# Optimization experiments

Hardware: AMD Instinct MI355X
Metric: run time of the kernel (lower is better)

## Reference

```python
import jax, jax.numpy as jnp
import numpy as np


def _chamfer(src, tgt):
    # src: [B, N, 3], tgt: [B, M, 3]
    x2 = jnp.sum(src * src, axis=-1)              # [B, N]
    y2 = jnp.sum(tgt * tgt, axis=-1)              # [B, M]
    xy = jnp.einsum('bnd,bmd->bnm', src, tgt)     # [B, N, M]
    d2 = x2[:, :, None] + y2[:, None, :] - 2.0 * xy
    d2 = jnp.maximum(d2, 0.0)                     # guard tiny negatives
    cham_x = jnp.min(d2, axis=2)                  # [B, N] min over tgt
    cham_y = jnp.min(d2, axis=1)                  # [B, M] min over src
    # point_reduction='mean', batch_reduction='sum'
    loss = jnp.sum(jnp.mean(cham_x, axis=1)) + jnp.sum(jnp.mean(cham_y, axis=1))
    return loss


def setup_inputs() -> dict:
    key = jax.random.key(0)
    k1, k2 = jax.random.split(key)
    src = jax.random.normal(k1, (16, 4096, 3), dtype=jnp.float32)
    tgt = jax.random.normal(k2, (16, 4096, 3), dtype=jnp.float32)
    return {"src": src, "tgt": tgt}


def reference(src, tgt):
    wgeo = 1.0
    return wgeo * _chamfer(src, tgt)
```

## Files before the change

### kernel.cpp

```cpp
#include <hip/hip_runtime.h>
#include <hip/hip_bf16.h>


#define BATCH   16
#define NPTS    4096
#define CHUNKC  1024
#define NCHUNKS (NPTS / CHUNKC)
#define NSTRIPS 16
#define NSTEP   (CHUNKC / 64)

typedef __attribute__((ext_vector_type(8)))  short short8;
typedef __attribute__((ext_vector_type(16))) float float16;

union U4S8 { uint4 u; short8 s; };

__device__ inline unsigned int bfb(float v) {
    __hip_bfloat16 h = __float2bfloat16(v);
    unsigned short u; __builtin_memcpy(&u, &h, 2);
    return (unsigned int)u;
}
__device__ inline float bff(float v) { return __bfloat162float(__float2bfloat16(v)); }

#define ONEB 0x3F80u

__device__ inline void buildA(float x, float y, float z, uint4& w0, uint4& w1) {
    float xhf = bff(x), yhf = bff(y), zhf = bff(z);
    float f = fmaf(x, x, fmaf(y, y, z * z));
    float fhf = bff(f);
    unsigned xh = bfb(xhf), yh = bfb(yhf), zh = bfb(zhf);
    unsigned xl = bfb(x - xhf), yl = bfb(y - yhf), zl = bfb(z - zhf);
    unsigned fh = bfb(fhf), fl = bfb(f - fhf);
    w0 = make_uint4(xh | (yh << 16), zh | (xh << 16),
                    yh | (zh << 16), xl | (yl << 16));
    w1 = make_uint4(zl | (fh << 16), fl | (ONEB << 16), ONEB, 0u);
}

__device__ inline void buildB(float x, float y, float z, uint4& w0, uint4& w1) {
    float xhf = bff(x), yhf = bff(y), zhf = bff(z);
    float f = fmaf(x, x, fmaf(y, y, z * z));
    float fhf = bff(f);
    unsigned a = bfb(-2.0f * xhf), b = bfb(-2.0f * yhf), c = bfb(-2.0f * zhf);
    unsigned d = bfb(-2.0f * (x - xhf)), e = bfb(-2.0f * (y - yhf)),
             g = bfb(-2.0f * (z - zhf));
    unsigned fh = bfb(fhf), fl = bfb(f - fhf);
    w0 = make_uint4(a | (b << 16), c | (d << 16),
                    e | (g << 16), a | (b << 16));
    w1 = make_uint4(c | (ONEB << 16), ONEB | (fh << 16), fl, 0u);
}

__global__ __launch_bounds__(256, 2) void chamfer_kernel(
    const float* __restrict__ src, const float* __restrict__ tgt,
    float* __restrict__ out)
{
    __shared__ uint4 sbuf[2][2][CHUNKC];
    __shared__ float wsum[4];

    int blk = blockIdx.x;
    const int strip = blk & (NSTRIPS - 1); blk >>= 4;
    const int b     = blk & 15;            blk >>= 4;
    const int dir   = blk;

    const int t    = threadIdx.x;
    const int lane = t & 63;
    const int w    = t >> 6;
    const int half = lane >> 5;
    const int l5   = lane & 31;

    const float* Araw = (dir ? tgt : src) + (size_t)b * NPTS * 3;
    const float* Braw = (dir ? src : tgt) + (size_t)b * NPTS * 3;

    short8 afr[2];
#pragma unroll
    for (int g = 0; g < 2; g++) {
        int row = strip * 256 + g * 128 + w * 32 + l5;
        uint4 w0, w1;
        buildA(Araw[3 * row], Araw[3 * row + 1], Araw[3 * row + 2], w0, w1);
        U4S8 tt; tt.u = half ? w1 : w0;
        afr[g] = tt.s;
    }

    float nx[4][3];
    auto loadRaw = [&](int c) {
#pragma unroll
        for (int k = 0; k < 4; k++) {
            int p = c * CHUNKC + t + k * 256;
            nx[k][0] = Braw[3 * p + 0];
            nx[k][1] = Braw[3 * p + 1];
            nx[k][2] = Braw[3 * p + 2];
        }
    };
    auto convertWrite = [&](int bi) {
#pragma unroll
        for (int k = 0; k < 4; k++) {
            int lp = t + k * 256;
            uint4 w0, w1;
            buildB(nx[k][0], nx[k][1], nx[k][2], w0, w1);
            sbuf[bi][0][lp] = w0;
            sbuf[bi][1][lp] = w1;
        }
    };

    const float16 z16 = {0.f,0.f,0.f,0.f,0.f,0.f,0.f,0.f,
                         0.f,0.f,0.f,0.f,0.f,0.f,0.f,0.f};
    float rm[2][16];
#pragma unroll
    for (int g = 0; g < 2; g++)
#pragma unroll
        for (int r = 0; r < 16; r++) rm[g][r] = 1e30f;

    loadRaw(0);
    convertWrite(0);
    for (int c = 0; c < NCHUNKS; c++) {
        __syncthreads();
        if (c + 1 < NCHUNKS) loadRaw(c + 1);
        const int bi = c & 1;

        U4S8 c0, c1, n0, n1;
        c0.u = sbuf[bi][half][l5];
        c1.u = sbuf[bi][half][32 + l5];
#pragma unroll 4
        for (int j2 = 0; j2 < NSTEP; j2++) {
            int nj = (j2 + 1) & (NSTEP - 1);
            n0.u = sbuf[bi][half][nj * 64 + l5];
            n1.u = sbuf[bi][half][nj * 64 + 32 + l5];
            float16 a00 = __builtin_amdgcn_mfma_f32_32x32x16_bf16(afr[0], c0.s, z16, 0, 0, 0);
            float16 a01 = __builtin_amdgcn_mfma_f32_32x32x16_bf16(afr[0], c1.s, z16, 0, 0, 0);
            float16 a10 = __builtin_amdgcn_mfma_f32_32x32x16_bf16(afr[1], c0.s, z16, 0, 0, 0);
            float16 a11 = __builtin_amdgcn_mfma_f32_32x32x16_bf16(afr[1], c1.s, z16, 0, 0, 0);
#pragma unroll
            for (int r = 0; r < 16; r++) {
                rm[0][r] = fminf(fminf(a00[r], a01[r]), rm[0][r]);
                rm[1][r] = fminf(fminf(a10[r], a11[r]), rm[1][r]);
            }
            c0 = n0; c1 = n1;
        }
        if (c + 1 < NCHUNKS) convertWrite((c + 1) & 1);
    }

#pragma unroll
    for (int mask = 1; mask <= 16; mask <<= 1)
#pragma unroll
        for (int g = 0; g < 2; g++)
#pragma unroll
            for (int r = 0; r < 16; r++)
                rm[g][r] = fminf(rm[g][r], __shfl_xor(rm[g][r], mask, 64));

    float s = 0.0f;
#pragma unroll
    for (int g = 0; g < 2; g++)
#pragma unroll
        for (int r = 0; r < 16; r++) s += fmaxf(rm[g][r], 0.0f);
    s += __shfl_xor(s, 32, 64);

    if (lane == 0) wsum[w] = s;
    __syncthreads();
    if (t == 0)
        atomicAdd(out, (wsum[0] + wsum[1] + wsum[2] + wsum[3]) * (1.0f / (float)NPTS));
}

extern "C" void kernel_launch(void* const* d_in, const int* in_sizes, int n_in,
                              void* d_out, int out_size, void* d_ws, size_t ws_size,
                              hipStream_t stream)
{
    const float* src = (const float*)d_in[0];
    const float* tgt = (const float*)d_in[1];
    float* out = (float*)d_out;

    hipMemsetAsync(out, 0, sizeof(float), stream);
    chamfer_kernel<<<2 * BATCH * NSTRIPS, 256, 0, stream>>>(src, tgt, out);
}
```

Measured before the change: 78.11 us.

## Precompute bf16-split B operands in a pre-pass and stage them via direct-to-LDS loads

A new pre-pass kernel converts every point of both clouds into its split-bf16 augmented B-operand encoding once and writes it to workspace; it also zeroes the output, replacing the memset. The main kernel then copies those prebuilt operands straight into LDS with global_load_lds, instead of loading raw xyz and rebuilding the encoding in every block. This removes the conversion ALU work that each of the 16 strips repeated, and the register staging of raw points. The cost is an extra kernel launch plus a few MB of workspace traffic, and correctness relies on the async LDS loads being complete at the barrier. The MFMA loop is also reordered by group, which is mostly cosmetic.

```diff
diff --git a/kernel.cpp b/kernel.cpp
--- a/kernel.cpp
+++ b/kernel.cpp
@@ -8,6 +8,7 @@
 #define NCHUNKS (NPTS / CHUNKC)
 #define NSTRIPS 16
 #define NSTEP   (CHUNKC / 64)
+#define NPER    (BATCH * NPTS)
 
 typedef __attribute__((ext_vector_type(8)))  short short8;
 typedef __attribute__((ext_vector_type(16))) float float16;
@@ -48,8 +49,27 @@
     w1 = make_uint4(c | (ONEB << 16), ONEB | (fh << 16), fl, 0u);
 }
 
+__global__ __launch_bounds__(256) void aug_kernel(
+    const float* __restrict__ src, const float* __restrict__ tgt,
+    uint4* __restrict__ Blo, uint4* __restrict__ Bhi, float* __restrict__ out)
+{
+    int i = blockIdx.x * 256 + threadIdx.x;
+    int role = i >> 16;
+    int p = i & (NPER - 1);
+    const float* base = role ? tgt : src;
+    float x = base[3 * p + 0];
+    float y = base[3 * p + 1];
+    float z = base[3 * p + 2];
+    uint4 w0, w1;
+    buildB(x, y, z, w0, w1);
+    Blo[i] = w0;
+    Bhi[i] = w1;
+    if (i == 0) out[0] = 0.0f;
+}
+
 __global__ __launch_bounds__(256, 2) void chamfer_kernel(
     const float* __restrict__ src, const float* __restrict__ tgt,
+    const uint4* __restrict__ Blo, const uint4* __restrict__ Bhi,
     float* __restrict__ out)
 {
     __shared__ uint4 sbuf[2][2][CHUNKC];
@@ -67,7 +87,7 @@
     const int l5   = lane & 31;
 
     const float* Araw = (dir ? tgt : src) + (size_t)b * NPTS * 3;
-    const float* Braw = (dir ? src : tgt) + (size_t)b * NPTS * 3;
+    const size_t Boff = (size_t)((dir ? 0 : 1) * BATCH + b) * NPTS;
 
     short8 afr[2];
 #pragma unroll
@@ -79,24 +99,18 @@
         afr[g] = tt.s;
     }
 
-    float nx[4][3];
-    auto loadRaw = [&](int c) {
+    auto stage = [&](int c, int bi) {
 #pragma unroll
-        for (int k = 0; k < 4; k++) {
-            int p = c * CHUNKC + t + k * 256;
-            nx[k][0] = Braw[3 * p + 0];
-            nx[k][1] = Braw[3 * p + 1];
-            nx[k][2] = Braw[3 * p + 2];
-        }
-    };
-    auto convertWrite = [&](int bi) {
+        for (int h = 0; h < 2; h++) {
+            const uint4* gbase = (h ? Bhi : Blo) + Boff + c * CHUNKC;
 #pragma unroll
-        for (int k = 0; k < 4; k++) {
-            int lp = t + k * 256;
-            uint4 w0, w1;
-            buildB(nx[k][0], nx[k][1], nx[k][2], w0, w1);
-            sbuf[bi][0][lp] = w0;
-            sbuf[bi][1][lp] = w1;
+            for (int j = 0; j < 4; j++) {
+                int li = w * 256 + j * 64;
+                __builtin_amdgcn_global_load_lds(
+                    (const __attribute__((address_space(1))) unsigned int*)(gbase + li + lane),
+                    (__attribute__((address_space(3))) unsigned int*)&sbuf[bi][h][li],
+                    16, 0, 0);
+            }
         }
     };
 
@@ -108,11 +122,10 @@
 #pragma unroll
         for (int r = 0; r < 16; r++) rm[g][r] = 1e30f;
 
-    loadRaw(0);
-    convertWrite(0);
+    stage(0, 0);
     for (int c = 0; c < NCHUNKS; c++) {
         __syncthreads();
-        if (c + 1 < NCHUNKS) loadRaw(c + 1);
+        if (c + 1 < NCHUNKS) stage(c + 1, (c + 1) & 1);
         const int bi = c & 1;
 
         U4S8 c0, c1, n0, n1;
@@ -123,18 +136,16 @@
             int nj = (j2 + 1) & (NSTEP - 1);
             n0.u = sbuf[bi][half][nj * 64 + l5];
             n1.u = sbuf[bi][half][nj * 64 + 32 + l5];
-            float16 a00 = __builtin_amdgcn_mfma_f32_32x32x16_bf16(afr[0], c0.s, z16, 0, 0, 0);
-            float16 a01 = __builtin_amdgcn_mfma_f32_32x32x16_bf16(afr[0], c1.s, z16, 0, 0, 0);
-            float16 a10 = __builtin_amdgcn_mfma_f32_32x32x16_bf16(afr[1], c0.s, z16, 0, 0, 0);
-            float16 a11 = __builtin_amdgcn_mfma_f32_32x32x16_bf16(afr[1], c1.s, z16, 0, 0, 0);
 #pragma unroll
-            for (int r = 0; r < 16; r++) {
-                rm[0][r] = fminf(fminf(a00[r], a01[r]), rm[0][r]);
-                rm[1][r] = fminf(fminf(a10[r], a11[r]), rm[1][r]);
+            for (int g = 0; g < 2; g++) {
+                float16 a0 = __builtin_amdgcn_mfma_f32_32x32x16_bf16(afr[g], c0.s, z16, 0, 0, 0);
+                float16 a1 = __builtin_amdgcn_mfma_f32_32x32x16_bf16(afr[g], c1.s, z16, 0, 0, 0);
+#pragma unroll
+                for (int r = 0; r < 16; r++)
+                    rm[g][r] = fminf(fminf(a0[r], a1[r]), rm[g][r]);
             }
             c0 = n0; c1 = n1;
         }
-        if (c + 1 < NCHUNKS) convertWrite((c + 1) & 1);
     }
 
 #pragma unroll
@@ -166,6 +177,9 @@
     const float* tgt = (const float*)d_in[1];
     float* out = (float*)d_out;
 
-    hipMemsetAsync(out, 0, sizeof(float), stream);
-    chamfer_kernel<<<2 * BATCH * NSTRIPS, 256, 0, stream>>>(src, tgt, out);
+    uint4* Blo = (uint4*)d_ws;
+    uint4* Bhi = Blo + 2 * NPER;
+
+    aug_kernel<<<2 * NPER / 256, 256, 0, stream>>>(src, tgt, Blo, Bhi, out);
+    chamfer_kernel<<<2 * BATCH * NSTRIPS, 256, 0, stream>>>(src, tgt, Blo, Bhi, out);
 }
```

Result: slower. 88.46 us (+13.3%).
